# Performance work log

Measured on AMD Instinct MI355X. Metric: run time of the kernel, lower is better.

## Reference

```python
import jax, jax.numpy as jnp
import numpy as np

VOCAB = 32000
DIM = 512
FFN = 4 * DIM
LAYERS_PER_BLOCK = [2, 2, 2]
THRESHOLDS = [3.5e-05, 4.0e-05, 1.0]
N_LAYERS = sum(LAYERS_PER_BLOCK)
B, S = 4, 1024


def setup_inputs() -> dict:
    key = jax.random.key(0)
    ks = jax.random.split(key, 8)
    x = jax.random.randint(ks[0], (B, S), 0, VOCAB)
    emb = jax.random.normal(ks[1], (VOCAB, DIM), jnp.float32) * 0.02
    head = jax.random.normal(ks[2], (VOCAB, DIM), jnp.float32) * (1.0 / np.sqrt(DIM))
    Wv = jax.random.normal(ks[3], (N_LAYERS, DIM, DIM), jnp.float32) * 0.02
    Wo = jax.random.normal(ks[4], (N_LAYERS, DIM, DIM), jnp.float32) * 0.02
    W1 = jax.random.normal(ks[5], (N_LAYERS, DIM, FFN), jnp.float32) * 0.02
    W2 = jax.random.normal(ks[6], (N_LAYERS, FFN, DIM), jnp.float32) * 0.02
    ln1_s = jnp.ones((N_LAYERS, DIM), jnp.float32)
    ln1_b = jnp.zeros((N_LAYERS, DIM), jnp.float32)
    ln2_s = jnp.ones((N_LAYERS, DIM), jnp.float32)
    ln2_b = jnp.zeros((N_LAYERS, DIM), jnp.float32)
    return {"x": x, "emb": emb, "head": head, "Wv": Wv, "Wo": Wo,
            "W1": W1, "W2": W2, "ln1_s": ln1_s, "ln1_b": ln1_b,
            "ln2_s": ln2_s, "ln2_b": ln2_b}


def _ln(x, s, b):
    m = jnp.mean(x, axis=-1, keepdims=True)
    v = jnp.mean((x - m) ** 2, axis=-1, keepdims=True)
    return (x - m) * jax.lax.rsqrt(v + 1e-5) * s + b


def reference(x, emb, head, Wv, Wo, W1, W2, ln1_s, ln1_b, ln2_s, ln2_b):
    T = B * S
    h = emb[x.reshape(-1)]                      # (T, dim) embedding gather
    active = jnp.ones((T,), dtype=bool)
    final_logits = jnp.zeros((T, VOCAB), jnp.float32)
    layer = 0
    n_blocks = len(LAYERS_PER_BLOCK)
    for b_idx, (n_l, thr) in enumerate(zip(LAYERS_PER_BLOCK, THRESHOLDS)):
        hb = h
        for l in range(layer, layer + n_l):
            # seq_len==1 attention: softmax over single key == 1 -> out = V @ Wo
            hn = _ln(hb, ln1_s[l], ln1_b[l])
            hb = hb + (hn @ Wv[l]) @ Wo[l]
            hn2 = _ln(hb, ln2_s[l], ln2_b[l])
            hb = hb + jax.nn.gelu(hn2 @ W1[l]) @ W2[l]
        layer += n_l
        logits = hb @ head.T                    # (T, vocab)
        conf = jnp.max(jax.nn.softmax(logits, axis=-1), axis=-1)
        is_last = b_idx == n_blocks - 1
        should_exit = conf > thr
        exit_now = active & (should_exit | is_last)   # scatter exiting tokens
        final_logits = jnp.where(exit_now[:, None], logits, final_logits)
        cont = active & ~exit_now
        h = jnp.where(cont[:, None], hb, h)           # only continuing tokens updated
        active = cont
    return final_logits.reshape(B, S, VOCAB)
```

## Files before the change

### kernel.cpp

```cpp
#include <hip/hip_runtime.h>
#include <hip/hip_bf16.h>
#include <math.h>

#define TT 4096
#define DIM 512
#define FFN 2048
#define NVOCAB 32000

typedef __attribute__((ext_vector_type(8))) short short8_t;
typedef __attribute__((ext_vector_type(4))) float f32x4;

__device__ __forceinline__ float gelu_f(float x) {
    float x3 = x * x * x;
    float u = 0.7978845608028654f * (x + 0.044715f * x3);
    return 0.5f * x * (1.0f + tanhf(u));
}

__device__ __forceinline__ unsigned short f2bf_rn(float f) {
    unsigned u = __float_as_uint(f);
    u += 0x7FFFu + ((u >> 16) & 1u);
    return (unsigned short)(u >> 16);
}

__global__ __launch_bounds__(128) void gather_kernel(const int* __restrict__ x,
                                                     const float* __restrict__ emb,
                                                     float* __restrict__ h,
                                                     int* __restrict__ flags) {
    int t = blockIdx.x;
    int idx = x[t];
    const float4 v = *(const float4*)&emb[(size_t)idx * DIM + threadIdx.x * 4];
    *(float4*)&h[(size_t)t * DIM + threadIdx.x * 4] = v;
    if (threadIdx.x == 0) flags[t] = 1;
}

__global__ __launch_bounds__(256) void cvt_hilo(const float* __restrict__ src,
                                                short* __restrict__ hi,
                                                short* __restrict__ lo, int n4) {
    int i = blockIdx.x * 256 + threadIdx.x;
    if (i >= n4) return;
    float4 v = *(const float4*)&src[(size_t)i * 4];
    float f[4] = {v.x, v.y, v.z, v.w};
    short4 hv, lv;
    short* hp = &hv.x;
    short* lp = &lv.x;
#pragma unroll
    for (int j = 0; j < 4; ++j) {
        unsigned short hb = f2bf_rn(f[j]);
        float hf = __uint_as_float((unsigned)hb << 16);
        unsigned short lb = f2bf_rn(f[j] - hf);
        hp[j] = (short)hb;
        lp[j] = (short)lb;
    }
    *(short4*)&hi[(size_t)i * 4] = hv;
    *(short4*)&lo[(size_t)i * 4] = lv;
}

__global__ __launch_bounds__(256) void cvt_bf16(const float* __restrict__ src,
                                                short* __restrict__ hi, int n4) {
    int i = blockIdx.x * 256 + threadIdx.x;
    if (i >= n4) return;
    float4 v = *(const float4*)&src[(size_t)i * 4];
    float f[4] = {v.x, v.y, v.z, v.w};
    short4 hv;
    short* hp = &hv.x;
#pragma unroll
    for (int j = 0; j < 4; ++j) hp[j] = (short)f2bf_rn(f[j]);
    *(short4*)&hi[(size_t)i * 4] = hv;
}

__global__ __launch_bounds__(256) void cvt_w_t(const float* __restrict__ W,
                                               short* __restrict__ hiT,
                                               short* __restrict__ loT,
                                               int K, int N) {
    __shared__ short hs[32][36];
    __shared__ short ls[32][36];
    const int n0 = blockIdx.x * 32, k0 = blockIdx.y * 32;
    const int r = threadIdx.x >> 3, c4 = (threadIdx.x & 7) << 2;
    float4 v = *(const float4*)&W[(size_t)(k0 + r) * N + n0 + c4];
    float f[4] = {v.x, v.y, v.z, v.w};
#pragma unroll
    for (int j = 0; j < 4; ++j) {
        unsigned short hb = f2bf_rn(f[j]);
        float hf = __uint_as_float((unsigned)hb << 16);
        unsigned short lb = f2bf_rn(f[j] - hf);
        hs[r][c4 + j] = (short)hb;
        ls[r][c4 + j] = (short)lb;
    }
    __syncthreads();
    const int nr = threadIdx.x >> 3, kc4 = (threadIdx.x & 7) << 2;
    short4 hv, lv;
    short* hp = &hv.x;
    short* lp = &lv.x;
#pragma unroll
    for (int j = 0; j < 4; ++j) {
        hp[j] = hs[kc4 + j][nr];
        lp[j] = ls[kc4 + j][nr];
    }
    *(short4*)&hiT[(size_t)(n0 + nr) * K + k0 + kc4] = hv;
    *(short4*)&loT[(size_t)(n0 + nr) * K + k0 + kc4] = lv;
}

template<bool IDX>
__global__ __launch_bounds__(256) void ln_kernel(const float* __restrict__ x,
                                                 const float* __restrict__ gam,
                                                 const float* __restrict__ bet,
                                                 float* __restrict__ out,
                                                 const int* __restrict__ idx,
                                                 const int* __restrict__ cnt) {
    int wv = threadIdx.x >> 6, lane = threadIdx.x & 63;
    int p = (blockIdx.x << 2) | wv;
    if (IDX && p >= *cnt) return;
    int t = IDX ? idx[p] : p;
    const float* row = x + (size_t)t * DIM;
    int base = lane * 8;
    float4 v0 = *(const float4*)&row[base];
    float4 v1 = *(const float4*)&row[base + 4];
    float s = v0.x + v0.y + v0.z + v0.w + v1.x + v1.y + v1.z + v1.w;
#pragma unroll
    for (int o = 32; o; o >>= 1) s += __shfl_xor(s, o, 64);
    float mean = s * (1.0f / (float)DIM);
    float d0 = v0.x - mean, d1 = v0.y - mean, d2 = v0.z - mean, d3 = v0.w - mean;
    float d4 = v1.x - mean, d5 = v1.y - mean, d6 = v1.z - mean, d7 = v1.w - mean;
    float q = d0*d0 + d1*d1 + d2*d2 + d3*d3 + d4*d4 + d5*d5 + d6*d6 + d7*d7;
#pragma unroll
    for (int o = 32; o; o >>= 1) q += __shfl_xor(q, o, 64);
    float var = q * (1.0f / (float)DIM);
    float rs = 1.0f / sqrtf(var + 1e-5f);
    float4 g0 = *(const float4*)&gam[base];
    float4 g1 = *(const float4*)&gam[base + 4];
    float4 b0 = *(const float4*)&bet[base];
    float4 b1 = *(const float4*)&bet[base + 4];
    float4 o0, o1;
    o0.x = d0 * rs * g0.x + b0.x;  o0.y = d1 * rs * g0.y + b0.y;
    o0.z = d2 * rs * g0.z + b0.z;  o0.w = d3 * rs * g0.w + b0.w;
    o1.x = d4 * rs * g1.x + b1.x;  o1.y = d5 * rs * g1.y + b1.y;
    o1.z = d6 * rs * g1.z + b1.z;  o1.w = d7 * rs * g1.w + b1.w;
    float* orow = out + (size_t)p * DIM;
    *(float4*)&orow[base] = o0;
    *(float4*)&orow[base + 4] = o1;
}

__global__ __launch_bounds__(256) void ln_hilo(const float* __restrict__ x,
                                               const float* __restrict__ gam,
                                               const float* __restrict__ bet,
                                               short* __restrict__ ohi,
                                               short* __restrict__ olo) {
    int wv = threadIdx.x >> 6, lane = threadIdx.x & 63;
    int t = (blockIdx.x << 2) | wv;
    const float* row = x + (size_t)t * DIM;
    int base = lane * 8;
    float4 v0 = *(const float4*)&row[base];
    float4 v1 = *(const float4*)&row[base + 4];
    float s = v0.x + v0.y + v0.z + v0.w + v1.x + v1.y + v1.z + v1.w;
#pragma unroll
    for (int o = 32; o; o >>= 1) s += __shfl_xor(s, o, 64);
    float mean = s * (1.0f / (float)DIM);
    float d[8] = {v0.x - mean, v0.y - mean, v0.z - mean, v0.w - mean,
                  v1.x - mean, v1.y - mean, v1.z - mean, v1.w - mean};
    float q = 0.0f;
#pragma unroll
    for (int j = 0; j < 8; ++j) q += d[j] * d[j];
#pragma unroll
    for (int o = 32; o; o >>= 1) q += __shfl_xor(q, o, 64);
    float var = q * (1.0f / (float)DIM);
    float rs = 1.0f / sqrtf(var + 1e-5f);
    float g[8], bb[8];
    *(float4*)&g[0] = *(const float4*)&gam[base];
    *(float4*)&g[4] = *(const float4*)&gam[base + 4];
    *(float4*)&bb[0] = *(const float4*)&bet[base];
    *(float4*)&bb[4] = *(const float4*)&bet[base + 4];
    short8_t hv, lv;
#pragma unroll
    for (int j = 0; j < 8; ++j) {
        float val = d[j] * rs * g[j] + bb[j];
        unsigned short hb = f2bf_rn(val);
        float hf = __uint_as_float((unsigned)hb << 16);
        hv[j] = (short)hb;
        lv[j] = (short)f2bf_rn(val - hf);
    }
    *(short8_t*)&ohi[(size_t)t * DIM + base] = hv;
    *(short8_t*)&olo[(size_t)t * DIM + base] = lv;
}

__device__ __forceinline__ void epi_store(int EPI, float val, size_t off,
                                          float* Cf, short* oHi, short* oLo) {
    if (EPI == 3) {
        Cf[off] = val;
    } else if (EPI == 2) {
        Cf[off] += val;
    } else if (EPI == 4) {
        float nv = Cf[off] + val;
        Cf[off] = nv;
        unsigned short hb = f2bf_rn(nv);
        float hf = __uint_as_float((unsigned)hb << 16);
        oHi[off] = (short)hb;
        oLo[off] = (short)f2bf_rn(nv - hf);
    } else {
        if (EPI == 1) val = gelu_f(val);
        unsigned short hb = f2bf_rn(val);
        float hf = __uint_as_float((unsigned)hb << 16);
        oHi[off] = (short)hb;
        oLo[off] = (short)f2bf_rn(val - hf);
    }
}

template<int EPI>
__global__ __launch_bounds__(256) void gemm_l_mfma(const short* __restrict__ Ah,
                                                   const short* __restrict__ Al,
                                                   const short* __restrict__ Bh,
                                                   const short* __restrict__ Bl,
                                                   float* __restrict__ Cf,
                                                   short* __restrict__ oHi,
                                                   short* __restrict__ oLo,
                                                   int N, int K) {
    __shared__ __align__(16) short sm[16384];
    short* sAh = sm;
    short* sAl = sm + 4096;
    short* sBh = sm + 8192;
    short* sBl = sm + 12288;
    const int tid = threadIdx.x;
    const int wv = tid >> 6, lane = tid & 63;
    const int m0 = blockIdx.x * 128;
    const int n0 = blockIdx.y * 128;
    const int wm = (wv & 1) * 64, wn = (wv >> 1) * 64;
    const int r16 = lane >> 2;
    const int gsw = ((lane & 3) ^ (r16 & 3)) << 3;
    const int fr = lane & 15;
    const int q = lane >> 4;

    f32x4 acc[4][4];
#pragma unroll
    for (int i = 0; i < 4; ++i)
#pragma unroll
        for (int j = 0; j < 4; ++j)
            acc[i][j] = (f32x4){0.0f, 0.0f, 0.0f, 0.0f};

    const int NKT = K >> 5;
    for (int kt = 0; kt < NKT; ++kt) {
        const int k0 = kt << 5;
        __syncthreads();
#pragma unroll
        for (int j = 0; j < 2; ++j) {
            const int rr = (wv << 5) + (j << 4);
            const int gr = rr + r16;
            const short* ga_h = Ah + (size_t)(m0 + gr) * K + k0 + gsw;
            const short* ga_l = Al + (size_t)(m0 + gr) * K + k0 + gsw;
            const short* gb_h = Bh + (size_t)(n0 + gr) * K + k0 + gsw;
            const short* gb_l = Bl + (size_t)(n0 + gr) * K + k0 + gsw;
            __builtin_amdgcn_global_load_lds((const __attribute__((address_space(1))) void*)ga_h,
                                             (__attribute__((address_space(3))) void*)(sAh + rr * 32), 16, 0, 0);
            __builtin_amdgcn_global_load_lds((const __attribute__((address_space(1))) void*)ga_l,
                                             (__attribute__((address_space(3))) void*)(sAl + rr * 32), 16, 0, 0);
            __builtin_amdgcn_global_load_lds((const __attribute__((address_space(1))) void*)gb_h,
                                             (__attribute__((address_space(3))) void*)(sBh + rr * 32), 16, 0, 0);
            __builtin_amdgcn_global_load_lds((const __attribute__((address_space(1))) void*)gb_l,
                                             (__attribute__((address_space(3))) void*)(sBl + rr * 32), 16, 0, 0);
        }
        __syncthreads();
        short8_t ah[4], al[4], bh[4], bl[4];
#pragma unroll
        for (int i = 0; i < 4; ++i) {
            const int ra = wm + i * 16 + fr;
            const int rb = wn + i * 16 + fr;
            const int swa = (q ^ (fr & 3)) << 3;
            ah[i] = *(const short8_t*)&sAh[ra * 32 + swa];
            al[i] = *(const short8_t*)&sAl[ra * 32 + swa];
            bh[i] = *(const short8_t*)&sBh[rb * 32 + swa];
            bl[i] = *(const short8_t*)&sBl[rb * 32 + swa];
        }
#pragma unroll
        for (int i = 0; i < 4; ++i)
#pragma unroll
            for (int j = 0; j < 4; ++j) {
                acc[i][j] = __builtin_amdgcn_mfma_f32_16x16x32_bf16(ah[i], bh[j], acc[i][j], 0, 0, 0);
                acc[i][j] = __builtin_amdgcn_mfma_f32_16x16x32_bf16(ah[i], bl[j], acc[i][j], 0, 0, 0);
                acc[i][j] = __builtin_amdgcn_mfma_f32_16x16x32_bf16(al[i], bh[j], acc[i][j], 0, 0, 0);
            }
    }
    const int row_base = (lane >> 4) << 2;
#pragma unroll
    for (int i = 0; i < 4; ++i)
#pragma unroll
        for (int j = 0; j < 4; ++j) {
            const int row = m0 + wm + i * 16 + row_base;
            const int col = n0 + wn + j * 16 + fr;
#pragma unroll
            for (int r = 0; r < 4; ++r)
                epi_store(EPI, acc[i][j][r], (size_t)(row + r) * N + col, Cf, oHi, oLo);
        }
}

template<int EPI>
__global__ __launch_bounds__(256) void gemm_l2(const short* __restrict__ Ah,
                                               const short* __restrict__ Al,
                                               const short* __restrict__ Bh,
                                               float* __restrict__ Cf,
                                               short* __restrict__ oHi,
                                               short* __restrict__ oLo,
                                               int N, int K) {
    __shared__ __align__(16) short sm[12288];
    short* sAh = sm;
    short* sAl = sm + 4096;
    short* sBh = sm + 8192;
    const int tid = threadIdx.x;
    const int wv = tid >> 6, lane = tid & 63;
    const int m0 = blockIdx.x * 128;
    const int n0 = blockIdx.y * 128;
    const int wm = (wv & 1) * 64, wn = (wv >> 1) * 64;
    const int r16 = lane >> 2;
    const int gsw = ((lane & 3) ^ (r16 & 3)) << 3;
    const int fr = lane & 15;
    const int q = lane >> 4;

    f32x4 acc[4][4];
#pragma unroll
    for (int i = 0; i < 4; ++i)
#pragma unroll
        for (int j = 0; j < 4; ++j)
            acc[i][j] = (f32x4){0.0f, 0.0f, 0.0f, 0.0f};

    const int NKT = K >> 5;
    for (int kt = 0; kt < NKT; ++kt) {
        const int k0 = kt << 5;
        __syncthreads();
#pragma unroll
        for (int j = 0; j < 2; ++j) {
            const int rr = (wv << 5) + (j << 4);
            const int gr = rr + r16;
            const short* ga_h = Ah + (size_t)(m0 + gr) * K + k0 + gsw;
            const short* ga_l = Al + (size_t)(m0 + gr) * K + k0 + gsw;
            const short* gb_h = Bh + (size_t)(n0 + gr) * K + k0 + gsw;
            __builtin_amdgcn_global_load_lds((const __attribute__((address_space(1))) void*)ga_h,
                                             (__attribute__((address_space(3))) void*)(sAh + rr * 32), 16, 0, 0);
            __builtin_amdgcn_global_load_lds((const __attribute__((address_space(1))) void*)ga_l,
                                             (__attribute__((address_space(3))) void*)(sAl + rr * 32), 16, 0, 0);
            __builtin_amdgcn_global_load_lds((const __attribute__((address_space(1))) void*)gb_h,
                                             (__attribute__((address_space(3))) void*)(sBh + rr * 32), 16, 0, 0);
        }
        __syncthreads();
        short8_t ah[4], al[4], bh[4];
#pragma unroll
        for (int i = 0; i < 4; ++i) {
            const int ra = wm + i * 16 + fr;
            const int rb = wn + i * 16 + fr;
            const int swa = (q ^ (fr & 3)) << 3;
            ah[i] = *(const short8_t*)&sAh[ra * 32 + swa];
            al[i] = *(const short8_t*)&sAl[ra * 32 + swa];
            bh[i] = *(const short8_t*)&sBh[rb * 32 + swa];
        }
#pragma unroll
        for (int i = 0; i < 4; ++i)
#pragma unroll
            for (int j = 0; j < 4; ++j) {
                acc[i][j] = __builtin_amdgcn_mfma_f32_16x16x32_bf16(ah[i], bh[j], acc[i][j], 0, 0, 0);
                acc[i][j] = __builtin_amdgcn_mfma_f32_16x16x32_bf16(al[i], bh[j], acc[i][j], 0, 0, 0);
            }
    }
    const int row_base = (lane >> 4) << 2;
#pragma unroll
    for (int i = 0; i < 4; ++i)
#pragma unroll
        for (int j = 0; j < 4; ++j) {
            const int row = m0 + wm + i * 16 + row_base;
            const int col = n0 + wn + j * 16 + fr;
#pragma unroll
            for (int r = 0; r < 4; ++r)
                epi_store(EPI, acc[i][j][r], (size_t)(row + r) * N + col, Cf, oHi, oLo);
        }
}

template<int EPI>
__global__ __launch_bounds__(256) void gemm_l64b(const short* __restrict__ Ah,
                                                 const short* __restrict__ Al,
                                                 const short* __restrict__ Bh,
                                                 float* __restrict__ Cf,
                                                 short* __restrict__ oHi,
                                                 short* __restrict__ oLo,
                                                 int N, int K) {
    __shared__ __align__(16) short sm[8192];
    short* sAh = sm;
    short* sAl = sm + 2048;
    short* sBh = sm + 4096;
    const int tid = threadIdx.x;
    const int wv = tid >> 6, lane = tid & 63;
    const int m0 = blockIdx.x * 64;
    const int n0 = blockIdx.y * 128;
    const int wm = (wv & 1) * 32, wn = (wv >> 1) * 64;
    const int r16 = lane >> 2;
    const int gsw = ((lane & 3) ^ (r16 & 3)) << 3;
    const int fr = lane & 15;
    const int q = lane >> 4;

    f32x4 acc[2][4];
#pragma unroll
    for (int i = 0; i < 2; ++i)
#pragma unroll
        for (int j = 0; j < 4; ++j)
            acc[i][j] = (f32x4){0.0f, 0.0f, 0.0f, 0.0f};

    const int NKT = K >> 5;
    for (int kt = 0; kt < NKT; ++kt) {
        const int k0 = kt << 5;
        __syncthreads();
        {
            const int rr = wv << 4;
            const int gr = rr + r16;
            const short* ga_h = Ah + (size_t)(m0 + gr) * K + k0 + gsw;
            const short* ga_l = Al + (size_t)(m0 + gr) * K + k0 + gsw;
            __builtin_amdgcn_global_load_lds((const __attribute__((address_space(1))) void*)ga_h,
                                             (__attribute__((address_space(3))) void*)(sAh + rr * 32), 16, 0, 0);
            __builtin_amdgcn_global_load_lds((const __attribute__((address_space(1))) void*)ga_l,
                                             (__attribute__((address_space(3))) void*)(sAl + rr * 32), 16, 0, 0);
        }
#pragma unroll
        for (int j = 0; j < 2; ++j) {
            const int rr = (wv << 5) + (j << 4);
            const int gr = rr + r16;
            const short* gb_h = Bh + (size_t)(n0 + gr) * K + k0 + gsw;
            __builtin_amdgcn_global_load_lds((const __attribute__((address_space(1))) void*)gb_h,
                                             (__attribute__((address_space(3))) void*)(sBh + rr * 32), 16, 0, 0);
        }
        __syncthreads();
        short8_t ah[2], al[2], bh[4];
        const int swa = (q ^ (fr & 3)) << 3;
#pragma unroll
        for (int i = 0; i < 2; ++i) {
            const int ra = wm + i * 16 + fr;
            ah[i] = *(const short8_t*)&sAh[ra * 32 + swa];
            al[i] = *(const short8_t*)&sAl[ra * 32 + swa];
        }
#pragma unroll
        for (int j = 0; j < 4; ++j) {
            const int rb = wn + j * 16 + fr;
            bh[j] = *(const short8_t*)&sBh[rb * 32 + swa];
        }
#pragma unroll
        for (int i = 0; i < 2; ++i)
#pragma unroll
            for (int j = 0; j < 4; ++j) {
                acc[i][j] = __builtin_amdgcn_mfma_f32_16x16x32_bf16(ah[i], bh[j], acc[i][j], 0, 0, 0);
                acc[i][j] = __builtin_amdgcn_mfma_f32_16x16x32_bf16(al[i], bh[j], acc[i][j], 0, 0, 0);
            }
    }
    const int row_base = (lane >> 4) << 2;
#pragma unroll
    for (int i = 0; i < 2; ++i)
#pragma unroll
        for (int j = 0; j < 4; ++j) {
            const int row = m0 + wm + i * 16 + row_base;
            const int col = n0 + wn + j * 16 + fr;
#pragma unroll
            for (int r = 0; r < 4; ++r)
                epi_store(EPI, acc[i][j][r], (size_t)(row + r) * N + col, Cf, oHi, oLo);
        }
}

template<int EPI>
__global__ __launch_bounds__(256) void gemm_l64(const short* __restrict__ Ah,
                                                const short* __restrict__ Al,
                                                const short* __restrict__ Bh,
                                                const short* __restrict__ Bl,
                                                float* __restrict__ Cf,
                                                short* __restrict__ oHi,
                                                short* __restrict__ oLo,
                                                int N, int K) {
    __shared__ __align__(16) short sm[12288];
    short* sAh = sm;
    short* sAl = sm + 2048;
    short* sBh = sm + 4096;
    short* sBl = sm + 8192;
    const int tid = threadIdx.x;
    const int wv = tid >> 6, lane = tid & 63;
    const int m0 = blockIdx.x * 64;
    const int n0 = blockIdx.y * 128;
    const int wm = (wv & 1) * 32, wn = (wv >> 1) * 64;
    const int r16 = lane >> 2;
    const int gsw = ((lane & 3) ^ (r16 & 3)) << 3;
    const int fr = lane & 15;
    const int q = lane >> 4;

    f32x4 acc[2][4];
#pragma unroll
    for (int i = 0; i < 2; ++i)
#pragma unroll
        for (int j = 0; j < 4; ++j)
            acc[i][j] = (f32x4){0.0f, 0.0f, 0.0f, 0.0f};

    const int NKT = K >> 5;
    for (int kt = 0; kt < NKT; ++kt) {
        const int k0 = kt << 5;
        __syncthreads();
        {
            const int rr = wv << 4;
            const int gr = rr + r16;
            const short* ga_h = Ah + (size_t)(m0 + gr) * K + k0 + gsw;
            const short* ga_l = Al + (size_t)(m0 + gr) * K + k0 + gsw;
            __builtin_amdgcn_global_load_lds((const __attribute__((address_space(1))) void*)ga_h,
                                             (__attribute__((address_space(3))) void*)(sAh + rr * 32), 16, 0, 0);
            __builtin_amdgcn_global_load_lds((const __attribute__((address_space(1))) void*)ga_l,
                                             (__attribute__((address_space(3))) void*)(sAl + rr * 32), 16, 0, 0);
        }
#pragma unroll
        for (int j = 0; j < 2; ++j) {
            const int rr = (wv << 5) + (j << 4);
            const int gr = rr + r16;
            const short* gb_h = Bh + (size_t)(n0 + gr) * K + k0 + gsw;
            const short* gb_l = Bl + (size_t)(n0 + gr) * K + k0 + gsw;
            __builtin_amdgcn_global_load_lds((const __attribute__((address_space(1))) void*)gb_h,
                                             (__attribute__((address_space(3))) void*)(sBh + rr * 32), 16, 0, 0);
            __builtin_amdgcn_global_load_lds((const __attribute__((address_space(1))) void*)gb_l,
                                             (__attribute__((address_space(3))) void*)(sBl + rr * 32), 16, 0, 0);
        }
        __syncthreads();
        short8_t ah[2], al[2], bh[4], bl[4];
        const int swa = (q ^ (fr & 3)) << 3;
#pragma unroll
        for (int i = 0; i < 2; ++i) {
            const int ra = wm + i * 16 + fr;
            ah[i] = *(const short8_t*)&sAh[ra * 32 + swa];
            al[i] = *(const short8_t*)&sAl[ra * 32 + swa];
        }
#pragma unroll
        for (int j = 0; j < 4; ++j) {
            const int rb = wn + j * 16 + fr;
            bh[j] = *(const short8_t*)&sBh[rb * 32 + swa];
            bl[j] = *(const short8_t*)&sBl[rb * 32 + swa];
        }
#pragma unroll
        for (int i = 0; i < 2; ++i)
#pragma unroll
            for (int j = 0; j < 4; ++j) {
                acc[i][j] = __builtin_amdgcn_mfma_f32_16x16x32_bf16(ah[i], bh[j], acc[i][j], 0, 0, 0);
                acc[i][j] = __builtin_amdgcn_mfma_f32_16x16x32_bf16(ah[i], bl[j], acc[i][j], 0, 0, 0);
                acc[i][j] = __builtin_amdgcn_mfma_f32_16x16x32_bf16(al[i], bh[j], acc[i][j], 0, 0, 0);
            }
    }
    const int row_base = (lane >> 4) << 2;
#pragma unroll
    for (int i = 0; i < 2; ++i)
#pragma unroll
        for (int j = 0; j < 4; ++j) {
            const int row = m0 + wm + i * 16 + row_base;
            const int col = n0 + wn + j * 16 + fr;
#pragma unroll
            for (int r = 0; r < 4; ++r)
                epi_store(EPI, acc[i][j][r], (size_t)(row + r) * N + col, Cf, oHi, oLo);
        }
}

__global__ __launch_bounds__(256) void gemm_head_bf16(const short* __restrict__ Ah,
                                                      const short* __restrict__ Bh,
                                                      float* __restrict__ C,
                                                      int N, int K) {
    __shared__ __align__(16) short sm[8192];
    short* sA = sm;
    short* sB = sm + 4096;
    const int tid = threadIdx.x;
    const int wv = tid >> 6, lane = tid & 63;
    const int m0 = blockIdx.x * 128;
    const int n0 = blockIdx.y * 128;
    const int wm = (wv & 1) * 64, wn = (wv >> 1) * 64;
    const int r16 = lane >> 2;
    const int gsw = ((lane & 3) ^ (r16 & 3)) << 3;
    const int fr = lane & 15;
    const int q = lane >> 4;

    f32x4 acc[4][4];
#pragma unroll
    for (int i = 0; i < 4; ++i)
#pragma unroll
        for (int j = 0; j < 4; ++j)
            acc[i][j] = (f32x4){0.0f, 0.0f, 0.0f, 0.0f};

    const int NKT = K >> 5;
    for (int kt = 0; kt < NKT; ++kt) {
        const int k0 = kt << 5;
        __syncthreads();
#pragma unroll
        for (int j = 0; j < 2; ++j) {
            const int rr = (wv << 5) + (j << 4);
            const int gr = rr + r16;
            const short* ga = Ah + (size_t)(m0 + gr) * K + k0 + gsw;
            const short* gb = Bh + (size_t)(n0 + gr) * K + k0 + gsw;
            __builtin_amdgcn_global_load_lds((const __attribute__((address_space(1))) void*)ga,
                                             (__attribute__((address_space(3))) void*)(sA + rr * 32), 16, 0, 0);
            __builtin_amdgcn_global_load_lds((const __attribute__((address_space(1))) void*)gb,
                                             (__attribute__((address_space(3))) void*)(sB + rr * 32), 16, 0, 0);
        }
        __syncthreads();
        short8_t ah[4], bh[4];
        const int swa = (q ^ (fr & 3)) << 3;
#pragma unroll
        for (int i = 0; i < 4; ++i) {
            ah[i] = *(const short8_t*)&sA[(wm + i * 16 + fr) * 32 + swa];
            bh[i] = *(const short8_t*)&sB[(wn + i * 16 + fr) * 32 + swa];
        }
#pragma unroll
        for (int i = 0; i < 4; ++i)
#pragma unroll
            for (int j = 0; j < 4; ++j)
                acc[i][j] = __builtin_amdgcn_mfma_f32_16x16x32_bf16(ah[i], bh[j], acc[i][j], 0, 0, 0);
    }
    const int row_base = (lane >> 4) << 2;
#pragma unroll
    for (int i = 0; i < 4; ++i)
#pragma unroll
        for (int j = 0; j < 4; ++j) {
            const int row = m0 + wm + i * 16 + row_base;
            const int col = n0 + wn + j * 16 + fr;
#pragma unroll
            for (int r = 0; r < 4; ++r)
                C[(size_t)(row + r) * N + col] = acc[i][j][r];
        }
}

template<bool ADD, bool GELU>
__global__ __launch_bounds__(256) void gemm_nn(const float* __restrict__ A,
                                               const float* __restrict__ B,
                                               float* __restrict__ C,
                                               int M, int N, int K) {
    const int m0 = blockIdx.y * 64, n0 = blockIdx.x * 64;
    __shared__ float As[16][68];
    __shared__ float Bs[16][68];
    const int tid = threadIdx.x;
    const int am = tid >> 2, ak = (tid & 3) << 2;
    const int bk = tid >> 4, bn = (tid & 15) << 2;
    const int tn = tid & 15, tm = tid >> 4;
    float acc[4][4] = {};
    for (int k0 = 0; k0 < K; k0 += 16) {
        float4 a4 = *(const float4*)&A[(size_t)(m0 + am) * K + k0 + ak];
        float4 b4 = *(const float4*)&B[(size_t)(k0 + bk) * N + n0 + bn];
        __syncthreads();
        As[ak + 0][am] = a4.x;
        As[ak + 1][am] = a4.y;
        As[ak + 2][am] = a4.z;
        As[ak + 3][am] = a4.w;
        *(float4*)&Bs[bk][bn] = b4;
        __syncthreads();
#pragma unroll
        for (int kk = 0; kk < 16; ++kk) {
            float4 av = *(const float4*)&As[kk][tm << 2];
            float4 bv = *(const float4*)&Bs[kk][tn << 2];
            float a[4] = {av.x, av.y, av.z, av.w};
            float b[4] = {bv.x, bv.y, bv.z, bv.w};
#pragma unroll
            for (int i = 0; i < 4; ++i)
#pragma unroll
                for (int j = 0; j < 4; ++j)
                    acc[i][j] = fmaf(a[i], b[j], acc[i][j]);
        }
    }
#pragma unroll
    for (int i = 0; i < 4; ++i) {
        size_t row = (size_t)(m0 + (tm << 2) + i);
        float* cp = &C[row * (size_t)N + n0 + (tn << 2)];
        float rr[4] = {acc[i][0], acc[i][1], acc[i][2], acc[i][3]};
        if (GELU) {
#pragma unroll
            for (int j = 0; j < 4; ++j) rr[j] = gelu_f(rr[j]);
        }
        if (ADD) {
            float4 cc = *(const float4*)cp;
            rr[0] += cc.x; rr[1] += cc.y; rr[2] += cc.z; rr[3] += cc.w;
        }
        float4 rv = {rr[0], rr[1], rr[2], rr[3]};
        *(float4*)cp = rv;
    }
}

template<bool ADD, bool GELU, bool SCAT>
__global__ __launch_bounds__(256) void gemm_nn_gs(const float* __restrict__ A,
                                                  const float* __restrict__ B,
                                                  float* __restrict__ C,
                                                  int N, int K,
                                                  const int* __restrict__ idx,
                                                  const int* __restrict__ cnt) {
    const int c = *cnt;
    const int ntm = (c + 63) >> 6;
    const int ntn = N >> 6;
    const int total = ntm * ntn;
    __shared__ float As[16][68];
    __shared__ float Bs[16][68];
    const int tid = threadIdx.x;
    const int am = tid >> 2, ak = (tid & 3) << 2;
    const int bk = tid >> 4, bn = (tid & 15) << 2;
    const int tn = tid & 15, tm = tid >> 4;
    for (int tile = blockIdx.x; tile < total; tile += gridDim.x) {
        const int m0 = (tile % ntm) << 6, n0 = (tile / ntm) << 6;
        int ar = m0 + am;
        ar = ar < c ? ar : c - 1;
        float acc[4][4] = {};
        for (int k0 = 0; k0 < K; k0 += 16) {
            float4 a4 = *(const float4*)&A[(size_t)ar * K + k0 + ak];
            float4 b4 = *(const float4*)&B[(size_t)(k0 + bk) * N + n0 + bn];
            __syncthreads();
            As[ak + 0][am] = a4.x;
            As[ak + 1][am] = a4.y;
            As[ak + 2][am] = a4.z;
            As[ak + 3][am] = a4.w;
            *(float4*)&Bs[bk][bn] = b4;
            __syncthreads();
#pragma unroll
            for (int kk = 0; kk < 16; ++kk) {
                float4 av = *(const float4*)&As[kk][tm << 2];
                float4 bv = *(const float4*)&Bs[kk][tn << 2];
                float a[4] = {av.x, av.y, av.z, av.w};
                float b[4] = {bv.x, bv.y, bv.z, bv.w};
#pragma unroll
                for (int i = 0; i < 4; ++i)
#pragma unroll
                    for (int j = 0; j < 4; ++j)
                        acc[i][j] = fmaf(a[i], b[j], acc[i][j]);
            }
        }
#pragma unroll
        for (int i = 0; i < 4; ++i) {
            int p = m0 + (tm << 2) + i;
            if (p >= c) continue;
            int r = SCAT ? idx[p] : p;
            float* cp = &C[(size_t)r * N + n0 + (tn << 2)];
            float rr[4] = {acc[i][0], acc[i][1], acc[i][2], acc[i][3]};
            if (GELU) {
#pragma unroll
                for (int j = 0; j < 4; ++j) rr[j] = gelu_f(rr[j]);
            }
            if (ADD) {
                float4 cc = *(const float4*)cp;
                rr[0] += cc.x; rr[1] += cc.y; rr[2] += cc.z; rr[3] += cc.w;
            }
            float4 rv = {rr[0], rr[1], rr[2], rr[3]};
            *(float4*)cp = rv;
        }
        __syncthreads();
    }
}

__global__ __launch_bounds__(256) void gemm_nt_head_gs(const float* __restrict__ A,
                                                       const float* __restrict__ Bt,
                                                       float* __restrict__ C,
                                                       const int* __restrict__ idx,
                                                       const int* __restrict__ cnt) {
    const int c = *cnt;
    const int ntm = (c + 63) >> 6;
    const int ntn = NVOCAB >> 6;
    const int total = ntm * ntn;
    __shared__ float As[16][68];
    __shared__ float Bs[16][68];
    const int tid = threadIdx.x;
    const int am = tid >> 2, ak = (tid & 3) << 2;
    const int tn = tid & 15, tm = tid >> 4;
    for (int tile = blockIdx.x; tile < total; tile += gridDim.x) {
        const int m0 = (tile % ntm) << 6, n0 = (tile / ntm) << 6;
        int ap = m0 + am;
        int ar = idx[ap < c ? ap : c - 1];
        float acc[4][4] = {};
        for (int k0 = 0; k0 < DIM; k0 += 16) {
            float4 a4 = *(const float4*)&A[(size_t)ar * DIM + k0 + ak];
            float4 b4 = *(const float4*)&Bt[(size_t)(n0 + am) * DIM + k0 + ak];
            __syncthreads();
            As[ak + 0][am] = a4.x;
            As[ak + 1][am] = a4.y;
            As[ak + 2][am] = a4.z;
            As[ak + 3][am] = a4.w;
            Bs[ak + 0][am] = b4.x;
            Bs[ak + 1][am] = b4.y;
            Bs[ak + 2][am] = b4.z;
            Bs[ak + 3][am] = b4.w;
            __syncthreads();
#pragma unroll
            for (int kk = 0; kk < 16; ++kk) {
                float4 av = *(const float4*)&As[kk][tm << 2];
                float4 bv = *(const float4*)&Bs[kk][tn << 2];
                float a[4] = {av.x, av.y, av.z, av.w};
                float b[4] = {bv.x, bv.y, bv.z, bv.w};
#pragma unroll
                for (int i = 0; i < 4; ++i)
#pragma unroll
                    for (int j = 0; j < 4; ++j)
                        acc[i][j] = fmaf(a[i], b[j], acc[i][j]);
            }
        }
#pragma unroll
        for (int i = 0; i < 4; ++i) {
            int p = m0 + (tm << 2) + i;
            if (p >= c) continue;
            int r = idx[p];
            float4 rv = {acc[i][0], acc[i][1], acc[i][2], acc[i][3]};
            *(float4*)&C[(size_t)r * NVOCAB + n0 + (tn << 2)] = rv;
        }
        __syncthreads();
    }
}

template<bool IDX>
__global__ __launch_bounds__(256) void conf_exit(const float* __restrict__ out,
                                                 int* __restrict__ flags,
                                                 const int* __restrict__ idx,
                                                 const int* __restrict__ cnt,
                                                 float thr) {
    int t;
    if (IDX) {
        if (blockIdx.x >= *cnt) return;
        t = idx[blockIdx.x];
    } else {
        t = blockIdx.x;
        if (flags[t] == 0) return;
    }
    const float4* row = (const float4*)(out + (size_t)t * NVOCAB);
    float m = -INFINITY, s = 0.0f;
    for (int i = threadIdx.x; i < NVOCAB / 4; i += 256) {
        float4 v = row[i];
        float m4 = fmaxf(fmaxf(v.x, v.y), fmaxf(v.z, v.w));
        float s4 = __expf(v.x - m4) + __expf(v.y - m4) + __expf(v.z - m4) + __expf(v.w - m4);
        if (m4 > m) {
            s = s * __expf(m - m4) + s4;
            m = m4;
        } else {
            s += s4 * __expf(m4 - m);
        }
    }
    __shared__ float ms[256], ss[256];
    ms[threadIdx.x] = m;
    ss[threadIdx.x] = s;
    __syncthreads();
    for (int st = 128; st; st >>= 1) {
        if (threadIdx.x < st) {
            float m1 = ms[threadIdx.x], s1 = ss[threadIdx.x];
            float m2 = ms[threadIdx.x + st], s2 = ss[threadIdx.x + st];
            float mm = fmaxf(m1, m2);
            ss[threadIdx.x] = s1 * __expf(m1 - mm) + s2 * __expf(m2 - mm);
            ms[threadIdx.x] = mm;
        }
        __syncthreads();
    }
    if (threadIdx.x == 0) {
        float conf = 1.0f / ss[0];
        if (conf > thr) flags[t] = 0;
    }
}

__global__ __launch_bounds__(256) void compact_kernel(const int* __restrict__ flags,
                                                      int* __restrict__ idx,
                                                      int* __restrict__ cnt) {
    __shared__ int wsum[4];
    __shared__ int base;
    if (threadIdx.x == 0) base = 0;
    int lane = threadIdx.x & 63, wv = threadIdx.x >> 6;
    for (int chunk = 0; chunk < TT; chunk += 256) {
        __syncthreads();
        int t = chunk + threadIdx.x;
        int f = flags[t];
        unsigned long long b = __ballot(f != 0);
        if (lane == 0) wsum[wv] = __popcll(b);
        __syncthreads();
        int off = base;
        for (int w = 0; w < wv; ++w) off += wsum[w];
        off += __popcll(b & ((1ull << lane) - 1));
        if (f) idx[off] = t;
        __syncthreads();
        if (threadIdx.x == 0) base += wsum[0] + wsum[1] + wsum[2] + wsum[3];
    }
    __syncthreads();
    if (threadIdx.x == 0) *cnt = base;
}

extern "C" void kernel_launch(void* const* d_in, const int* in_sizes, int n_in,
                              void* d_out, int out_size, void* d_ws, size_t ws_size,
                              hipStream_t stream) {
    const int* x = (const int*)d_in[0];
    const float* emb = (const float*)d_in[1];
    const float* head = (const float*)d_in[2];
    const float* Wv = (const float*)d_in[3];
    const float* Wo = (const float*)d_in[4];
    const float* W1 = (const float*)d_in[5];
    const float* W2 = (const float*)d_in[6];
    const float* ln1s = (const float*)d_in[7];
    const float* ln1b = (const float*)d_in[8];
    const float* ln2s = (const float*)d_in[9];
    const float* ln2b = (const float*)d_in[10];
    float* out = (float*)d_out;
    float* ws = (float*)d_ws;

    float* h  = ws;
    float* hn = ws + 2097152;
    float* tA = ws + 4194304;
    float* tF = ws + 6291456;
    short* hnHi = (short*)hn;
    short* hnLo = hnHi + TT * DIM;
    short* tAHi = (short*)tA;
    short* tALo = tAHi + TT * DIM;
    short* tFHi = (short*)tF;
    short* tFLo = tFHi + TT * FFN;
    int* flags = (int*)(ws + 14680064);
    int* idxl  = flags + TT;
    int* cntp  = flags + 2 * TT;
    short* hHi    = (short*)(ws + 14700000);
    short* hLo    = (short*)(ws + 15748576);
    short* headHi = (short*)(ws + 16797152);
    short* headLo = (short*)(ws + 24989152);
    short* wT     = (short*)(ws + 33181152);
    const size_t LSTRIDE = 5242880;
    const size_t NEED_T2 = (size_t)33181152 * 4;
    const size_t NEED_T1 = (size_t)38424032 * 4;
    const int tier = ws_size >= NEED_T1 ? 1 : (ws_size >= NEED_T2 ? 2 : 3);

    gather_kernel<<<TT, 128, 0, stream>>>(x, emb, h, flags);

    const float THR[3] = {3.5e-05f, 4.0e-05f, 1.0f};
    const dim3 gDD(DIM / 64, TT / 64), gDF(FFN / 64, TT / 64), gHead(NVOCAB / 64, TT / 64);

    if (tier == 1) {
        for (int l = 0; l < 2; ++l) {
            short* wb = wT + (size_t)l * LSTRIDE;
            cvt_hilo<<<(DIM * DIM / 4 + 255) / 256, 256, 0, stream>>>(Wv + (size_t)l * DIM * DIM, tAHi, tALo, DIM * DIM / 4);
            cvt_w_t<<<dim3(DIM / 32, DIM / 32), 256, 0, stream>>>(Wo + (size_t)l * DIM * DIM, wb + 524288, wb + 786432, DIM, DIM);
            gemm_l64<0><<<dim3(DIM / 64, DIM / 128), 256, 0, stream>>>(
                wb + 524288, wb + 786432, tAHi, tALo, nullptr, wb, wb + 262144, DIM, DIM);
            cvt_w_t<<<dim3(FFN / 32, DIM / 32), 256, 0, stream>>>(W1 + (size_t)l * DIM * FFN, wb + 1048576, wb + 2097152, DIM, FFN);
            cvt_w_t<<<dim3(DIM / 32, FFN / 32), 256, 0, stream>>>(W2 + (size_t)l * FFN * DIM, wb + 3145728, wb + 4194304, FFN, DIM);
        }
        for (int l = 0; l < 2; ++l) {
            short* wb = wT + (size_t)l * LSTRIDE;
            ln_hilo<<<TT / 4, 256, 0, stream>>>(h, ln1s + l * DIM, ln1b + l * DIM, hnHi, hnLo);
            gemm_l64b<2><<<dim3(TT / 64, DIM / 128), 256, 0, stream>>>(hnHi, hnLo, wb, h, nullptr, nullptr, DIM, DIM);
            ln_hilo<<<TT / 4, 256, 0, stream>>>(h, ln2s + l * DIM, ln2b + l * DIM, hnHi, hnLo);
            gemm_l2<1><<<dim3(TT / 128, FFN / 128), 256, 0, stream>>>(hnHi, hnLo, wb + 1048576, nullptr, tFHi, tFLo, FFN, DIM);
            if (l == 1) {
                gemm_l64b<4><<<dim3(TT / 64, DIM / 128), 256, 0, stream>>>(tFHi, tFLo, wb + 3145728, h, hHi, hLo, DIM, FFN);
            } else {
                gemm_l64b<2><<<dim3(TT / 64, DIM / 128), 256, 0, stream>>>(tFHi, tFLo, wb + 3145728, h, nullptr, nullptr, DIM, FFN);
            }
        }
        cvt_bf16<<<(NVOCAB * DIM / 4 + 255) / 256, 256, 0, stream>>>(head, headHi, NVOCAB * DIM / 4);
        gemm_head_bf16<<<dim3(TT / 128, NVOCAB / 128), 256, 0, stream>>>(hHi, headHi, out, NVOCAB, DIM);
        conf_exit<false><<<TT, 256, 0, stream>>>(out, flags, nullptr, nullptr, THR[0]);
    } else {
        for (int l = 0; l < 2; ++l) {
            ln_kernel<false><<<TT / 4, 256, 0, stream>>>(h, ln1s + l * DIM, ln1b + l * DIM, hn, nullptr, nullptr);
            gemm_nn<false, false><<<gDD, 256, 0, stream>>>(hn, Wv + (size_t)l * DIM * DIM, tA, TT, DIM, DIM);
            gemm_nn<true, false><<<gDD, 256, 0, stream>>>(tA, Wo + (size_t)l * DIM * DIM, h, TT, DIM, DIM);
            ln_kernel<false><<<TT / 4, 256, 0, stream>>>(h, ln2s + l * DIM, ln2b + l * DIM, hn, nullptr, nullptr);
            gemm_nn<false, true><<<gDF, 256, 0, stream>>>(hn, W1 + (size_t)l * DIM * FFN, tF, TT, FFN, DIM);
            gemm_nn<true, false><<<gDD, 256, 0, stream>>>(tF, W2 + (size_t)l * FFN * DIM, h, TT, DIM, FFN);
        }
        if (tier == 2) {
            cvt_hilo<<<(TT * DIM / 4 + 255) / 256, 256, 0, stream>>>(h, hHi, hLo, TT * DIM / 4);
            cvt_hilo<<<(NVOCAB * DIM / 4 + 255) / 256, 256, 0, stream>>>(head, headHi, headLo, NVOCAB * DIM / 4);
            gemm_l_mfma<3><<<dim3(TT / 128, NVOCAB / 128), 256, 0, stream>>>(hHi, hLo, headHi, headLo, out, nullptr, nullptr, NVOCAB, DIM);
        } else {
            compact_kernel<<<1, 256, 0, stream>>>(flags, idxl, cntp);
            gemm_nt_head_gs<<<512, 256, 0, stream>>>(h, head, out, idxl, cntp);
        }
        conf_exit<false><<<TT, 256, 0, stream>>>(out, flags, nullptr, nullptr, THR[0]);
    }
    compact_kernel<<<1, 256, 0, stream>>>(flags, idxl, cntp);

    for (int b = 1; b < 3; ++b) {
        for (int li = 0; li < 2; ++li) {
            int l = b * 2 + li;
            ln_kernel<true><<<TT / 4, 256, 0, stream>>>(h, ln1s + l * DIM, ln1b + l * DIM, hn, idxl, cntp);
            gemm_nn_gs<false, false, false><<<256, 256, 0, stream>>>(hn, Wv + (size_t)l * DIM * DIM, tA, DIM, DIM, idxl, cntp);
            gemm_nn_gs<true, false, true><<<256, 256, 0, stream>>>(tA, Wo + (size_t)l * DIM * DIM, h, DIM, DIM, idxl, cntp);
            ln_kernel<true><<<TT / 4, 256, 0, stream>>>(h, ln2s + l * DIM, ln2b + l * DIM, hn, idxl, cntp);
            gemm_nn_gs<false, true, false><<<256, 256, 0, stream>>>(hn, W1 + (size_t)l * DIM * FFN, tF, FFN, DIM, idxl, cntp);
            gemm_nn_gs<true, false, true><<<256, 256, 0, stream>>>(tF, W2 + (size_t)l * FFN * DIM, h, DIM, FFN, idxl, cntp);
        }
        gemm_nt_head_gs<<<512, 256, 0, stream>>>(h, head, out, idxl, cntp);
        if (b == 1) {
            conf_exit<true><<<TT, 256, 0, stream>>>(out, flags, idxl, cntp, THR[1]);
            compact_kernel<<<1, 256, 0, stream>>>(flags, idxl, cntp);
        }
    }
}
```

Measured before the change: 742.1 us.

## Fuse softmax partial max/sum into head GEMM epilogue and drop unused lo weight conversion

The head GEMM epilogue now computes a per-row, per-64-column-group max and sum of exponentials through wave shuffles and writes these partials to a small buffer. A new conf_reduce kernel merges the partials with an online-softmax combine to get the confidence and set exit flags. This replaces conf_exit, which re-read the full 4096x32000 logits tensor. Separately, W1 and W2 transposes now write only the bf16 high part, since the lo half appears unused by the FFN GEMMs. The cost is extra epilogue work and exp calls in the head GEMM.

```diff
diff --git a/kernel.cpp b/kernel.cpp
--- a/kernel.cpp
+++ b/kernel.cpp
@@ -6,6 +6,7 @@
 #define DIM 512
 #define FFN 2048
 #define NVOCAB 32000
+#define NGRP 500
 
 typedef __attribute__((ext_vector_type(8))) short short8_t;
 typedef __attribute__((ext_vector_type(4))) float f32x4;
@@ -98,6 +99,25 @@
     }
     *(short4*)&hiT[(size_t)(n0 + nr) * K + k0 + kc4] = hv;
     *(short4*)&loT[(size_t)(n0 + nr) * K + k0 + kc4] = lv;
+}
+
+__global__ __launch_bounds__(256) void cvt_w_t_hi(const float* __restrict__ W,
+                                                  short* __restrict__ hiT,
+                                                  int K, int N) {
+    __shared__ short hs[32][36];
+    const int n0 = blockIdx.x * 32, k0 = blockIdx.y * 32;
+    const int r = threadIdx.x >> 3, c4 = (threadIdx.x & 7) << 2;
+    float4 v = *(const float4*)&W[(size_t)(k0 + r) * N + n0 + c4];
+    float f[4] = {v.x, v.y, v.z, v.w};
+#pragma unroll
+    for (int j = 0; j < 4; ++j) hs[r][c4 + j] = (short)f2bf_rn(f[j]);
+    __syncthreads();
+    const int nr = threadIdx.x >> 3, kc4 = (threadIdx.x & 7) << 2;
+    short4 hv;
+    short* hp = &hv.x;
+#pragma unroll
+    for (int j = 0; j < 4; ++j) hp[j] = hs[kc4 + j][nr];
+    *(short4*)&hiT[(size_t)(n0 + nr) * K + k0 + kc4] = hv;
 }
 
 template<bool IDX>
@@ -551,6 +571,7 @@
 __global__ __launch_bounds__(256) void gemm_head_bf16(const short* __restrict__ Ah,
                                                       const short* __restrict__ Bh,
                                                       float* __restrict__ C,
+                                                      float2* __restrict__ pp,
                                                       int N, int K) {
     __shared__ __align__(16) short sm[8192];
     short* sA = sm;
@@ -559,6 +580,7 @@
     const int wv = tid >> 6, lane = tid & 63;
     const int m0 = blockIdx.x * 128;
     const int n0 = blockIdx.y * 128;
+    const int nt = blockIdx.y;
     const int wm = (wv & 1) * 64, wn = (wv >> 1) * 64;
     const int r16 = lane >> 2;
     const int gsw = ((lane & 3) ^ (r16 & 3)) << 3;
@@ -601,7 +623,24 @@
             for (int j = 0; j < 4; ++j)
                 acc[i][j] = __builtin_amdgcn_mfma_f32_16x16x32_bf16(ah[i], bh[j], acc[i][j], 0, 0, 0);
     }
-    const int row_base = (lane >> 4) << 2;
+    const int hi = lane >> 4;
+    const int row_base = hi << 2;
+#pragma unroll
+    for (int i = 0; i < 4; ++i)
+#pragma unroll
+        for (int r = 0; r < 4; ++r) {
+            float v0 = acc[i][0][r], v1 = acc[i][1][r];
+            float v2 = acc[i][2][r], v3 = acc[i][3][r];
+            float mg = fmaxf(fmaxf(v0, v1), fmaxf(v2, v3));
+#pragma unroll
+            for (int o = 1; o < 16; o <<= 1) mg = fmaxf(mg, __shfl_xor(mg, o, 64));
+            float sg = __expf(v0 - mg) + __expf(v1 - mg) + __expf(v2 - mg) + __expf(v3 - mg);
+#pragma unroll
+            for (int o = 1; o < 16; o <<= 1) sg += __shfl_xor(sg, o, 64);
+            if (fr == 0)
+                pp[(size_t)(m0 + wm + i * 16 + hi * 4 + r) * NGRP + nt * 2 + (wn >> 6)] =
+                    make_float2(mg, sg);
+        }
 #pragma unroll
     for (int i = 0; i < 4; ++i)
 #pragma unroll
@@ -612,6 +651,31 @@
             for (int r = 0; r < 4; ++r)
                 C[(size_t)(row + r) * N + col] = acc[i][j][r];
         }
+}
+
+__global__ __launch_bounds__(256) void conf_reduce(const float2* __restrict__ pp,
+                                                   int* __restrict__ flags, float thr) {
+    int wv = threadIdx.x >> 6, lane = threadIdx.x & 63;
+    int t = blockIdx.x * 4 + wv;
+    float m = -INFINITY, s = 0.0f;
+    for (int k = lane; k < NGRP; k += 64) {
+        float2 v = pp[(size_t)t * NGRP + k];
+        float mm = fmaxf(m, v.x);
+        s = s * __expf(m - mm) + v.y * __expf(v.x - mm);
+        m = mm;
+    }
+#pragma unroll
+    for (int o = 1; o < 64; o <<= 1) {
+        float mo = __shfl_xor(m, o, 64);
+        float so = __shfl_xor(s, o, 64);
+        float mm = fmaxf(m, mo);
+        s = s * __expf(m - mm) + so * __expf(mo - mm);
+        m = mm;
+    }
+    if (lane == 0) {
+        float conf = 1.0f / s;
+        if (conf > thr) flags[t] = 0;
+    }
 }
 
 template<bool ADD, bool GELU>
@@ -891,6 +955,7 @@
     short* tALo = tAHi + TT * DIM;
     short* tFHi = (short*)tF;
     short* tFLo = tFHi + TT * FFN;
+    float2* pp = (float2*)tF;
     int* flags = (int*)(ws + 14680064);
     int* idxl  = flags + TT;
     int* cntp  = flags + 2 * TT;
@@ -916,8 +981,8 @@
             cvt_w_t<<<dim3(DIM / 32, DIM / 32), 256, 0, stream>>>(Wo + (size_t)l * DIM * DIM, wb + 524288, wb + 786432, DIM, DIM);
             gemm_l64<0><<<dim3(DIM / 64, DIM / 128), 256, 0, stream>>>(
                 wb + 524288, wb + 786432, tAHi, tALo, nullptr, wb, wb + 262144, DIM, DIM);
-            cvt_w_t<<<dim3(FFN / 32, DIM / 32), 256, 0, stream>>>(W1 + (size_t)l * DIM * FFN, wb + 1048576, wb + 2097152, DIM, FFN);
-            cvt_w_t<<<dim3(DIM / 32, FFN / 32), 256, 0, stream>>>(W2 + (size_t)l * FFN * DIM, wb + 3145728, wb + 4194304, FFN, DIM);
+            cvt_w_t_hi<<<dim3(FFN / 32, DIM / 32), 256, 0, stream>>>(W1 + (size_t)l * DIM * FFN, wb + 1048576, DIM, FFN);
+            cvt_w_t_hi<<<dim3(DIM / 32, FFN / 32), 256, 0, stream>>>(W2 + (size_t)l * FFN * DIM, wb + 3145728, FFN, DIM);
         }
         for (int l = 0; l < 2; ++l) {
             short* wb = wT + (size_t)l * LSTRIDE;
@@ -932,8 +997,8 @@
             }
         }
         cvt_bf16<<<(NVOCAB * DIM / 4 + 255) / 256, 256, 0, stream>>>(head, headHi, NVOCAB * DIM / 4);
-        gemm_head_bf16<<<dim3(TT / 128, NVOCAB / 128), 256, 0, stream>>>(hHi, headHi, out, NVOCAB, DIM);
-        conf_exit<false><<<TT, 256, 0, stream>>>(out, flags, nullptr, nullptr, THR[0]);
+        gemm_head_bf16<<<dim3(TT / 128, NVOCAB / 128), 256, 0, stream>>>(hHi, headHi, out, pp, NVOCAB, DIM);
+        conf_reduce<<<TT / 4, 256, 0, stream>>>(pp, flags, THR[0]);
     } else {
         for (int l = 0; l < 2; ++l) {
             ln_kernel<false><<<TT / 4, 256, 0, stream>>>(h, ln1s + l * DIM, ln1b + l * DIM, hn, nullptr, nullptr);
```

New measurement: 686.7 us. -7.5%, faster.
